# Performance work log

Measured on AMD Instinct MI355X. Metric: run time of the kernel, lower is better.

Reference implementation:

```python
import jax, jax.numpy as jnp
import numpy as np

N_NODES = 100000
N_EDGES = 3200000
IN_DIM = 128
HIDDEN = 64
N_GRAPHS = 512


def setup_inputs() -> dict:
    key = jax.random.key(0)
    k1, k2, k3, k4, k5, k6, k7, k8 = jax.random.split(key, 8)
    x = jax.random.normal(k1, (N_NODES, IN_DIM), dtype=jnp.float32)
    edge_index = jax.random.randint(k2, (2, N_EDGES), 0, N_NODES, dtype=jnp.int64)
    batch = jnp.sort(jax.random.randint(k3, (N_NODES,), 0, N_GRAPHS, dtype=jnp.int64))
    # Glorot-style init for GCNConv weights, zero bias (PyG default)
    s1 = 1.0 / np.sqrt(IN_DIM)
    s2 = 1.0 / np.sqrt(HIDDEN)
    W1 = jax.random.uniform(k4, (IN_DIM, HIDDEN), jnp.float32, -s1, s1)
    b1 = jnp.zeros((HIDDEN,), jnp.float32)
    W2 = jax.random.uniform(k5, (HIDDEN, HIDDEN), jnp.float32, -s2, s2)
    b2 = jnp.zeros((HIDDEN,), jnp.float32)
    return {"x": x, "W1": W1, "b1": b1, "W2": W2, "b2": b2,
            "edge_index": edge_index, "batch": batch}


def _gcn_conv(x, src, dst, W, b, n_nodes):
    # PyG GCNConv: h = x W;  out_i = sum_j norm_ij * h_j + b
    # with self-loops added and norm = deg^{-1/2}[src] * deg^{-1/2}[dst]
    h = x @ W  # [N, out]
    deg = jax.ops.segment_sum(jnp.ones_like(dst, dtype=h.dtype), dst,
                              num_segments=n_nodes)  # in-degree incl. self-loops
    dis = jnp.where(deg > 0, jax.lax.rsqrt(jnp.maximum(deg, 1e-12)), 0.0)
    norm = dis[src] * dis[dst]                      # [E+N]
    msg = h[src] * norm[:, None]                    # gather + scale
    out = jax.ops.segment_sum(msg, dst, num_segments=n_nodes)  # scatter-add
    return out + b


def reference(x, W1, b1, W2, b2, edge_index, batch):
    n = x.shape[0]
    loops = jnp.arange(n, dtype=edge_index.dtype)
    src = jnp.concatenate([edge_index[0], loops])
    dst = jnp.concatenate([edge_index[1], loops])
    h = jax.nn.relu(_gcn_conv(x, src, dst, W1, b1, n))
    h = jax.nn.relu(_gcn_conv(h, src, dst, W2, b2, n))
    # global_mean_pool over batch ids
    sums = jax.ops.segment_sum(h, batch, num_segments=N_GRAPHS)
    cnts = jax.ops.segment_sum(jnp.ones((n,), h.dtype), batch,
                               num_segments=N_GRAPHS)
    return sums / jnp.maximum(cnts, 1.0)[:, None]
```

## Files before the change

### kernel.cpp

```cpp
#include <hip/hip_runtime.h>
#include <hip/hip_bf16.h>

#define N_NODES 100000
#define N_EDGES 3200000
#define IN_DIM 128
#define HIDDEN 64
#define N_GRAPHS 512

#define NB 196
#define NPB 512
#define P1B 512
#define SEGC 80
#define BCAP2 18432

typedef __hip_bfloat16 bf16;
__device__ __forceinline__ float b2f(bf16 v) { return __bfloat162float(v); }

__global__ __launch_bounds__(512) void bin_kernel(const int* __restrict__ src,
                                                  const int* __restrict__ dst,
                                                  int* __restrict__ gcnt,
                                                  int* __restrict__ btot,
                                                  unsigned* __restrict__ slab) {
    __shared__ int lcnt[NB];
    int t = threadIdx.x, blk = blockIdx.x;
    if (t < NB) lcnt[t] = 0;
    __syncthreads();
    const int EPB = (N_EDGES + P1B - 1) / P1B;
    long e0 = (long)blk * EPB;
    long e1 = e0 + EPB; if (e1 > N_EDGES) e1 = N_EDGES;
    unsigned* ms = slab + (size_t)blk * NB * SEGC;
    for (long e = e0 + t; e < e1; e += 512) {
        int d = dst[e];
        unsigned p = ((unsigned)src[e] << 9) | (unsigned)(d & (NPB - 1));
        int bb = d >> 9;
        int pos = atomicAdd(&lcnt[bb], 1);
        if (pos < SEGC) ms[bb * SEGC + pos] = p;
    }
    __syncthreads();
    if (t < NB) {
        int c = lcnt[t]; if (c > SEGC) c = SEGC;
        gcnt[blk * NB + t] = c;
        atomicAdd(&btot[t], c);
    }
}

__global__ __launch_bounds__(256) void bstart_kernel(const int* __restrict__ btot,
                                                     int* __restrict__ bstart) {
    __shared__ int s[NB];
    int t = threadIdx.x;
    if (t < NB) s[t] = btot[t];
    __syncthreads();
    for (int off = 1; off < NB; off <<= 1) {
        int u = (t < NB && t >= off) ? s[t - off] : 0;
        __syncthreads();
        if (t < NB) s[t] += u;
        __syncthreads();
    }
    if (t < NB) bstart[t + 1] = s[t];
    if (t == 0) bstart[0] = 0;
}

__global__ __launch_bounds__(1024) void csr_sort_kernel(
        const unsigned* __restrict__ slab, const int* __restrict__ gcnt,
        const int* __restrict__ bstart, int2* __restrict__ be,
        float* __restrict__ dis, int* __restrict__ csr) {
    __shared__ int cnt[NPB], sc[NPB], lb[NPB], cur[NPB];
    __shared__ int stmp[P1B];
    __shared__ int segoff[P1B + 1];
    __shared__ unsigned ebuf[BCAP2];
    int b = blockIdx.x, t = threadIdx.x;
    if (t < P1B) stmp[t] = gcnt[t * NB + b];
    __syncthreads();
    for (int off = 1; off < P1B; off <<= 1) {
        int u = 0;
        if (t < P1B && t >= off) u = stmp[t - off];
        __syncthreads();
        if (t < P1B) stmp[t] += u;
        __syncthreads();
    }
    if (t < P1B) segoff[t + 1] = stmp[t];
    if (t == 0) segoff[0] = 0;
    __syncthreads();
    int ec = segoff[P1B];
    if (ec > BCAP2) ec = BCAP2;
    int w = t >> 6, lane = t & 63;
    for (int s = w; s < P1B; s += 16) {
        int o = segoff[s];
        int c = segoff[s + 1] - o;
        const unsigned* sp = slab + ((size_t)s * NB + b) * SEGC;
        for (int i = lane; i < c; i += 64)
            if (o + i < BCAP2) ebuf[o + i] = sp[i];
    }
    if (t < NPB) cnt[t] = 0;
    __syncthreads();
    for (int i = t; i < ec; i += 1024)
        atomicAdd(&cnt[(int)(ebuf[i] & (NPB - 1))], 1);
    __syncthreads();
    int v = (t < NPB) ? cnt[t] : 0;
    if (t < NPB) sc[t] = v;
    __syncthreads();
    for (int off = 1; off < NPB; off <<= 1) {
        int u = (t < NPB && t >= off) ? sc[t - off] : 0;
        __syncthreads();
        if (t < NPB) sc[t] += u;
        __syncthreads();
    }
    if (t < NPB) { lb[t] = sc[t] - v; cur[t] = 0; }
    __syncthreads();
    int gb0 = bstart[b];
    for (int i = t; i < ec; i += 1024) {
        unsigned p = ebuf[i];
        int dl = (int)(p & (NPB - 1));
        int k = atomicAdd(&cur[dl], 1);
        csr[gb0 + lb[dl] + k] = (int)(p >> 9);
    }
    int n0 = b * NPB;
    int nn = N_NODES - n0; if (nn > NPB) nn = NPB;
    if (t < nn) {
        int n = n0 + t;
        int bg = gb0 + lb[t];
        be[n] = make_int2(bg, bg + cnt[t]);
        dis[n] = rsqrtf((float)(cnt[t] + 1));
    }
}

template <int K>
__global__ __launch_bounds__(256) void gemm_kernel(
        const float* __restrict__ in, const float* __restrict__ W,
        const float* __restrict__ dis, bf16* __restrict__ hd) {
    int tid = threadIdx.x;
    int lane = tid & 63;
    float Wr[K];
    #pragma unroll
    for (int k = 0; k < K; ++k) Wr[k] = W[k * HIDDEN + lane];
    int w = __builtin_amdgcn_readfirstlane(tid >> 6);
    int wave = blockIdx.x * 4 + w;
    int nw = gridDim.x * 4;
    for (int n0 = wave * 4; n0 < N_NODES; n0 += nw * 4) {
        const float* xr = in + (size_t)n0 * K;
        float a0 = 0.f, a1 = 0.f, a2 = 0.f, a3 = 0.f;
        #pragma unroll
        for (int k = 0; k < K; ++k) {
            float wv = Wr[k];
            a0 = fmaf(xr[k],         wv, a0);
            a1 = fmaf(xr[K + k],     wv, a1);
            a2 = fmaf(xr[2 * K + k], wv, a2);
            a3 = fmaf(xr[3 * K + k], wv, a3);
        }
        bf16* o = hd + (size_t)n0 * HIDDEN + lane;
        o[0]          = __float2bfloat16(a0 * dis[n0]);
        o[HIDDEN]     = __float2bfloat16(a1 * dis[n0 + 1]);
        o[2 * HIDDEN] = __float2bfloat16(a2 * dis[n0 + 2]);
        o[3 * HIDDEN] = __float2bfloat16(a3 * dis[n0 + 3]);
    }
}

template <int POOL>
__global__ __launch_bounds__(256) void pull_kernel(
        const bf16* __restrict__ hd, const float* __restrict__ dis,
        const int2* __restrict__ be, const int* __restrict__ csr,
        const float* __restrict__ bias,
        float* __restrict__ act,
        const int* __restrict__ batch, float* __restrict__ pool,
        float* __restrict__ cnt) {
    int w = threadIdx.x >> 6, lane = threadIdx.x & 63;
    int wid = blockIdx.x * 4 + w;
    int nwaves = gridDim.x * 4;
    int per = (N_NODES + nwaves - 1) / nwaves;
    int n0 = wid * per;
    int n1 = n0 + per; if (n1 > N_NODES) n1 = N_NODES;
    for (int node = n0; node < n1; ++node) {
        int2 r = be[node];
        int beg = r.x, end = r.y;
        float a0 = 0.f, a1 = 0.f, a2 = 0.f, a3 = 0.f;
        for (int j = beg; j < end; j += 64) {
            int rem = end - j;
            int m = rem < 64 ? rem : 64;
            int idx = (lane < m) ? __builtin_nontemporal_load(&csr[j + lane]) : 0;
            int t = 0;
            for (; t + 8 <= m; t += 8) {
                int s0 = __shfl(idx, t);
                int s1 = __shfl(idx, t + 1);
                int s2 = __shfl(idx, t + 2);
                int s3 = __shfl(idx, t + 3);
                int s4 = __shfl(idx, t + 4);
                int s5 = __shfl(idx, t + 5);
                int s6 = __shfl(idx, t + 6);
                int s7 = __shfl(idx, t + 7);
                float v0 = b2f(hd[(size_t)s0 * HIDDEN + lane]);
                float v1 = b2f(hd[(size_t)s1 * HIDDEN + lane]);
                float v2 = b2f(hd[(size_t)s2 * HIDDEN + lane]);
                float v3 = b2f(hd[(size_t)s3 * HIDDEN + lane]);
                float v4 = b2f(hd[(size_t)s4 * HIDDEN + lane]);
                float v5 = b2f(hd[(size_t)s5 * HIDDEN + lane]);
                float v6 = b2f(hd[(size_t)s6 * HIDDEN + lane]);
                float v7 = b2f(hd[(size_t)s7 * HIDDEN + lane]);
                a0 += v0 + v4;
                a1 += v1 + v5;
                a2 += v2 + v6;
                a3 += v3 + v7;
            }
            for (; t < m; ++t) {
                int s = __shfl(idx, t);
                a0 += b2f(hd[(size_t)s * HIDDEN + lane]);
            }
        }
        float acc = (a0 + a1) + (a2 + a3);
        float self = b2f(hd[(size_t)node * HIDDEN + lane]);
        float row = dis[node] * (acc + self) + bias[lane];
        float v = row > 0.f ? row : 0.f;
        if (POOL == 0) {
            act[(size_t)node * HIDDEN + lane] = v;
        } else {
            int g = batch[node];
            atomicAdd(&pool[g * HIDDEN + lane], v);
            if (lane == 0) atomicAdd(&cnt[g], 1.0f);
        }
    }
}

__global__ void final_kernel(const float* __restrict__ pool,
                             const float* __restrict__ cnt,
                             float* __restrict__ out) {
    int i = blockIdx.x * blockDim.x + threadIdx.x;
    if (i < N_GRAPHS * HIDDEN) {
        float c = cnt[i >> 6];
        c = c > 1.0f ? c : 1.0f;
        out[i] = pool[i] / c;
    }
}

extern "C" void kernel_launch(void* const* d_in, const int* in_sizes, int n_in,
                              void* d_out, int out_size, void* d_ws, size_t ws_size,
                              hipStream_t stream) {
    const float* x  = (const float*)d_in[0];
    const float* W1 = (const float*)d_in[1];
    const float* b1 = (const float*)d_in[2];
    const float* W2 = (const float*)d_in[3];
    const float* b2 = (const float*)d_in[4];
    const int* edge_index = (const int*)d_in[5];
    const int* batch      = (const int*)d_in[6];
    float* out = (float*)d_out;
    (void)in_sizes; (void)n_in; (void)out_size; (void)ws_size;

    char* ws = (char*)d_ws;
    int*      gcnt   = (int*)     (ws + 0);
    int*      btot   = (int*)     (ws + 401408);
    int*      bstart = (int*)     (ws + 402432);
    float*    pool   = (float*)   (ws + 403456);
    float*    cnt    = (float*)   (ws + 534528);
    int2*     be     = (int2*)    (ws + 536576);
    float*    dis    = (float*)   (ws + 1336576);
    unsigned* slab   = (unsigned*)(ws + 1736704);
    float*    act    = (float*)   (ws + 1736704);
    int*      csr    = (int*)     (ws + 33849344);
    bf16*     hd     = (bf16*)    (ws + 46649344);

    const int* srcv = edge_index;
    const int* dstv = edge_index + N_EDGES;

    hipMemsetAsync(ws, 0, 536576, stream);

    bin_kernel<<<P1B, 512, 0, stream>>>(srcv, dstv, gcnt, btot, slab);
    bstart_kernel<<<1, 256, 0, stream>>>(btot, bstart);
    csr_sort_kernel<<<NB, 1024, 0, stream>>>(slab, gcnt, bstart, be, dis, csr);

    gemm_kernel<IN_DIM><<<1024, 256, 0, stream>>>(x, W1, dis, hd);
    pull_kernel<0><<<2048, 256, 0, stream>>>(hd, dis, be, csr, b1,
                                             act, nullptr, nullptr, nullptr);

    gemm_kernel<HIDDEN><<<1024, 256, 0, stream>>>(act, W2, dis, hd);
    pull_kernel<1><<<2048, 256, 0, stream>>>(hd, dis, be, csr, b2,
                                             nullptr, batch, pool, cnt);

    final_kernel<<<(N_GRAPHS * HIDDEN + 255) / 256, 256, 0, stream>>>(pool, cnt, out);
}
```

Measured before the change: 460.6 us.

## Fuse second-layer weight matmul into first GCN aggregation kernel

The first aggregation kernel now applies ReLU and then multiplies each node's row by W2, held in shared memory, using cross-lane readlane broadcasts. It writes the deg-scaled bf16 features for layer two directly. This eliminates the fp32 activation buffer write/read and the separate second GEMM launch. In exchange it adds per-node dot-product work and LDS usage to a gather-bound kernel, which may reduce occupancy.

Measured after the change: 486.7 us. 1.06x slower.

```diff
diff --git a/kernel.cpp b/kernel.cpp
--- a/kernel.cpp
+++ b/kernel.cpp
@@ -15,6 +15,9 @@
 
 typedef __hip_bfloat16 bf16;
 __device__ __forceinline__ float b2f(bf16 v) { return __bfloat162float(v); }
+__device__ __forceinline__ float rlane(float v, int k) {
+    return __int_as_float(__builtin_amdgcn_readlane(__float_as_int(v), k));
+}
 
 __global__ __launch_bounds__(512) void bin_kernel(const int* __restrict__ src,
                                                   const int* __restrict__ dst,
@@ -155,15 +158,17 @@
     }
 }
 
-template <int POOL>
-__global__ __launch_bounds__(256) void pull_kernel(
+__global__ __launch_bounds__(256) void pull_fused_kernel(
         const bf16* __restrict__ hd, const float* __restrict__ dis,
         const int2* __restrict__ be, const int* __restrict__ csr,
-        const float* __restrict__ bias,
-        float* __restrict__ act,
-        const int* __restrict__ batch, float* __restrict__ pool,
-        float* __restrict__ cnt) {
-    int w = threadIdx.x >> 6, lane = threadIdx.x & 63;
+        const float* __restrict__ bias, const float* __restrict__ W2,
+        bf16* __restrict__ hd2) {
+    __shared__ float W2s[HIDDEN * HIDDEN];
+    int t = threadIdx.x;
+    for (int i = t; i < HIDDEN * HIDDEN; i += 256) W2s[i] = W2[i];
+    __syncthreads();
+    int w = t >> 6, lane = t & 63;
+    float bl = bias[lane];
     int wid = blockIdx.x * 4 + w;
     int nwaves = gridDim.x * 4;
     int per = (N_NODES + nwaves - 1) / nwaves;
@@ -177,16 +182,16 @@
             int rem = end - j;
             int m = rem < 64 ? rem : 64;
             int idx = (lane < m) ? __builtin_nontemporal_load(&csr[j + lane]) : 0;
-            int t = 0;
-            for (; t + 8 <= m; t += 8) {
-                int s0 = __shfl(idx, t);
-                int s1 = __shfl(idx, t + 1);
-                int s2 = __shfl(idx, t + 2);
-                int s3 = __shfl(idx, t + 3);
-                int s4 = __shfl(idx, t + 4);
-                int s5 = __shfl(idx, t + 5);
-                int s6 = __shfl(idx, t + 6);
-                int s7 = __shfl(idx, t + 7);
+            int t8 = 0;
+            for (; t8 + 8 <= m; t8 += 8) {
+                int s0 = __shfl(idx, t8);
+                int s1 = __shfl(idx, t8 + 1);
+                int s2 = __shfl(idx, t8 + 2);
+                int s3 = __shfl(idx, t8 + 3);
+                int s4 = __shfl(idx, t8 + 4);
+                int s5 = __shfl(idx, t8 + 5);
+                int s6 = __shfl(idx, t8 + 6);
+                int s7 = __shfl(idx, t8 + 7);
                 float v0 = b2f(hd[(size_t)s0 * HIDDEN + lane]);
                 float v1 = b2f(hd[(size_t)s1 * HIDDEN + lane]);
                 float v2 = b2f(hd[(size_t)s2 * HIDDEN + lane]);
@@ -200,22 +205,80 @@
                 a2 += v2 + v6;
                 a3 += v3 + v7;
             }
-            for (; t < m; ++t) {
-                int s = __shfl(idx, t);
+            for (; t8 < m; ++t8) {
+                int s = __shfl(idx, t8);
+                a0 += b2f(hd[(size_t)s * HIDDEN + lane]);
+            }
+        }
+        float acc = (a0 + a1) + (a2 + a3);
+        float dn = dis[node];
+        float self = b2f(hd[(size_t)node * HIDDEN + lane]);
+        float row = dn * (acc + self) + bl;
+        float v = row > 0.f ? row : 0.f;
+        float g2 = 0.f;
+        #pragma unroll
+        for (int k = 0; k < HIDDEN; ++k)
+            g2 = fmaf(rlane(v, k), W2s[k * HIDDEN + lane], g2);
+        hd2[(size_t)node * HIDDEN + lane] = __float2bfloat16(g2 * dn);
+    }
+}
+
+__global__ __launch_bounds__(256) void pull_pool_kernel(
+        const bf16* __restrict__ hd, const float* __restrict__ dis,
+        const int2* __restrict__ be, const int* __restrict__ csr,
+        const float* __restrict__ bias,
+        const int* __restrict__ batch, float* __restrict__ pool,
+        float* __restrict__ cnt) {
+    int w = threadIdx.x >> 6, lane = threadIdx.x & 63;
+    float bl = bias[lane];
+    int wid = blockIdx.x * 4 + w;
+    int nwaves = gridDim.x * 4;
+    int per = (N_NODES + nwaves - 1) / nwaves;
+    int n0 = wid * per;
+    int n1 = n0 + per; if (n1 > N_NODES) n1 = N_NODES;
+    for (int node = n0; node < n1; ++node) {
+        int2 r = be[node];
+        int beg = r.x, end = r.y;
+        float a0 = 0.f, a1 = 0.f, a2 = 0.f, a3 = 0.f;
+        for (int j = beg; j < end; j += 64) {
+            int rem = end - j;
+            int m = rem < 64 ? rem : 64;
+            int idx = (lane < m) ? __builtin_nontemporal_load(&csr[j + lane]) : 0;
+            int t8 = 0;
+            for (; t8 + 8 <= m; t8 += 8) {
+                int s0 = __shfl(idx, t8);
+                int s1 = __shfl(idx, t8 + 1);
+                int s2 = __shfl(idx, t8 + 2);
+                int s3 = __shfl(idx, t8 + 3);
+                int s4 = __shfl(idx, t8 + 4);
+                int s5 = __shfl(idx, t8 + 5);
+                int s6 = __shfl(idx, t8 + 6);
+                int s7 = __shfl(idx, t8 + 7);
+                float v0 = b2f(hd[(size_t)s0 * HIDDEN + lane]);
+                float v1 = b2f(hd[(size_t)s1 * HIDDEN + lane]);
+                float v2 = b2f(hd[(size_t)s2 * HIDDEN + lane]);
+                float v3 = b2f(hd[(size_t)s3 * HIDDEN + lane]);
+                float v4 = b2f(hd[(size_t)s4 * HIDDEN + lane]);
+                float v5 = b2f(hd[(size_t)s5 * HIDDEN + lane]);
+                float v6 = b2f(hd[(size_t)s6 * HIDDEN + lane]);
+                float v7 = b2f(hd[(size_t)s7 * HIDDEN + lane]);
+                a0 += v0 + v4;
+                a1 += v1 + v5;
+                a2 += v2 + v6;
+                a3 += v3 + v7;
+            }
+            for (; t8 < m; ++t8) {
+                int s = __shfl(idx, t8);
                 a0 += b2f(hd[(size_t)s * HIDDEN + lane]);
             }
         }
         float acc = (a0 + a1) + (a2 + a3);
         float self = b2f(hd[(size_t)node * HIDDEN + lane]);
-        float row = dis[node] * (acc + self) + bias[lane];
+        float row = dis[node] * (acc + self) + bl;
         float v = row > 0.f ? row : 0.f;
-        if (POOL == 0) {
-            act[(size_t)node * HIDDEN + lane] = v;
-        } else {
-            int g = batch[node];
-            atomicAdd(&pool[g * HIDDEN + lane], v);
-            if (lane == 0) atomicAdd(&cnt[g], 1.0f);
-        }
+        int g = batch[node];
+        atomicAdd(&pool[g * HIDDEN + lane], v);
+        if (lane == 0) atomicAdd(&cnt[g], 1.0f);
     }
 }
 
@@ -252,9 +315,9 @@
     int2*     be     = (int2*)    (ws + 536576);
     float*    dis    = (float*)   (ws + 1336576);
     unsigned* slab   = (unsigned*)(ws + 1736704);
-    float*    act    = (float*)   (ws + 1736704);
+    bf16*     hd1    = (bf16*)    (ws + 1736704);
     int*      csr    = (int*)     (ws + 33849344);
-    bf16*     hd     = (bf16*)    (ws + 46649344);
+    bf16*     hd2    = (bf16*)    (ws + 46649344);
 
     const int* srcv = edge_index;
     const int* dstv = edge_index + N_EDGES;
@@ -265,13 +328,10 @@
     bstart_kernel<<<1, 256, 0, stream>>>(btot, bstart);
     csr_sort_kernel<<<NB, 1024, 0, stream>>>(slab, gcnt, bstart, be, dis, csr);
 
-    gemm_kernel<IN_DIM><<<1024, 256, 0, stream>>>(x, W1, dis, hd);
-    pull_kernel<0><<<2048, 256, 0, stream>>>(hd, dis, be, csr, b1,
-                                             act, nullptr, nullptr, nullptr);
-
-    gemm_kernel<HIDDEN><<<1024, 256, 0, stream>>>(act, W2, dis, hd);
-    pull_kernel<1><<<2048, 256, 0, stream>>>(hd, dis, be, csr, b2,
-                                             nullptr, batch, pool, cnt);
+    gemm_kernel<IN_DIM><<<1024, 256, 0, stream>>>(x, W1, dis, hd1);
+    pull_fused_kernel<<<2048, 256, 0, stream>>>(hd1, dis, be, csr, b1, W2, hd2);
+    pull_pool_kernel<<<2048, 256, 0, stream>>>(hd2, dis, be, csr, b2,
+                                               batch, pool, cnt);
 
     final_kernel<<<(N_GRAPHS * HIDDEN + 255) / 256, 256, 0, stream>>>(pool, cnt, out);
 }
```

## Split pull-kernel feature columns into two halves, each wave-half gathering alternate edges

Applied to the files above, without the earlier changes.

The pull aggregation now covers the 64 feature columns in two passes of 32. In each pass, the two 32-lane halves of a wave gather different neighbor edges at once and combine their sums with a cross-half shuffle. Each gather instruction therefore fetches two 64-byte bf16 row segments instead of one 128-byte row, which shrinks each pass's working set of hd and may improve L2 cache hit rates. In exchange, every node's CSR indices and row metadata are read twice, the instruction count roughly doubles, and each load moves less contiguous data.

After: 567.5 us. +23.2%, slower.

```diff
diff --git a/kernel.cpp b/kernel.cpp
--- a/kernel.cpp
+++ b/kernel.cpp
@@ -164,57 +164,75 @@
         const int* __restrict__ batch, float* __restrict__ pool,
         float* __restrict__ cnt) {
     int w = threadIdx.x >> 6, lane = threadIdx.x & 63;
+    int slot = lane >> 5;
+    int sub  = lane & 31;
     int wid = blockIdx.x * 4 + w;
     int nwaves = gridDim.x * 4;
     int per = (N_NODES + nwaves - 1) / nwaves;
     int n0 = wid * per;
     int n1 = n0 + per; if (n1 > N_NODES) n1 = N_NODES;
-    for (int node = n0; node < n1; ++node) {
-        int2 r = be[node];
-        int beg = r.x, end = r.y;
-        float a0 = 0.f, a1 = 0.f, a2 = 0.f, a3 = 0.f;
-        for (int j = beg; j < end; j += 64) {
-            int rem = end - j;
-            int m = rem < 64 ? rem : 64;
-            int idx = (lane < m) ? __builtin_nontemporal_load(&csr[j + lane]) : 0;
-            int t = 0;
-            for (; t + 8 <= m; t += 8) {
-                int s0 = __shfl(idx, t);
-                int s1 = __shfl(idx, t + 1);
-                int s2 = __shfl(idx, t + 2);
-                int s3 = __shfl(idx, t + 3);
-                int s4 = __shfl(idx, t + 4);
-                int s5 = __shfl(idx, t + 5);
-                int s6 = __shfl(idx, t + 6);
-                int s7 = __shfl(idx, t + 7);
-                float v0 = b2f(hd[(size_t)s0 * HIDDEN + lane]);
-                float v1 = b2f(hd[(size_t)s1 * HIDDEN + lane]);
-                float v2 = b2f(hd[(size_t)s2 * HIDDEN + lane]);
-                float v3 = b2f(hd[(size_t)s3 * HIDDEN + lane]);
-                float v4 = b2f(hd[(size_t)s4 * HIDDEN + lane]);
-                float v5 = b2f(hd[(size_t)s5 * HIDDEN + lane]);
-                float v6 = b2f(hd[(size_t)s6 * HIDDEN + lane]);
-                float v7 = b2f(hd[(size_t)s7 * HIDDEN + lane]);
-                a0 += v0 + v4;
-                a1 += v1 + v5;
-                a2 += v2 + v6;
-                a3 += v3 + v7;
+    for (int half = 0; half < 2; ++half) {
+        int fb = half * 32;
+        for (int node = n0; node < n1; ++node) {
+            int2 r = be[node];
+            int beg = r.x, end = r.y;
+            float a0 = 0.f, a1 = 0.f, a2 = 0.f, a3 = 0.f;
+            for (int j = beg; j < end; j += 64) {
+                int rem = end - j;
+                int m = rem < 64 ? rem : 64;
+                int idx = (lane < m) ? __builtin_nontemporal_load(&csr[j + lane]) : 0;
+                int t = 0;
+                for (; t + 16 <= m; t += 16) {
+                    int s0 = __shfl(idx, t + slot);
+                    int s1 = __shfl(idx, t + 2 + slot);
+                    int s2 = __shfl(idx, t + 4 + slot);
+                    int s3 = __shfl(idx, t + 6 + slot);
+                    int s4 = __shfl(idx, t + 8 + slot);
+                    int s5 = __shfl(idx, t + 10 + slot);
+                    int s6 = __shfl(idx, t + 12 + slot);
+                    int s7 = __shfl(idx, t + 14 + slot);
+                    float v0 = b2f(hd[(size_t)s0 * HIDDEN + fb + sub]);
+                    float v1 = b2f(hd[(size_t)s1 * HIDDEN + fb + sub]);
+                    float v2 = b2f(hd[(size_t)s2 * HIDDEN + fb + sub]);
+                    float v3 = b2f(hd[(size_t)s3 * HIDDEN + fb + sub]);
+                    float v4 = b2f(hd[(size_t)s4 * HIDDEN + fb + sub]);
+                    float v5 = b2f(hd[(size_t)s5 * HIDDEN + fb + sub]);
+                    float v6 = b2f(hd[(size_t)s6 * HIDDEN + fb + sub]);
+                    float v7 = b2f(hd[(size_t)s7 * HIDDEN + fb + sub]);
+                    a0 += v0 + v4;
+                    a1 += v1 + v5;
+                    a2 += v2 + v6;
+                    a3 += v3 + v7;
+                }
+                if (t < m) {
+                    #pragma unroll
+                    for (int u = 0; u < 8; ++u) {
+                        int eb = t + 2 * u;
+                        if (eb < m) {
+                            int e = eb + slot;
+                            int ee = e < 64 ? e : 63;
+                            int s = __shfl(idx, ee);
+                            float vv = b2f(hd[(size_t)s * HIDDEN + fb + sub]);
+                            if (e < m) a0 += vv;
+                        }
+                    }
+                }
             }
-            for (; t < m; ++t) {
-                int s = __shfl(idx, t);
-                a0 += b2f(hd[(size_t)s * HIDDEN + lane]);
+            float acc = (a0 + a1) + (a2 + a3);
+            acc += __shfl_xor(acc, 32);
+            float self = b2f(hd[(size_t)node * HIDDEN + fb + sub]);
+            float row = dis[node] * (acc + self) + bias[fb + sub];
+            float v = row > 0.f ? row : 0.f;
+            if (POOL == 0) {
+                if (slot == 0)
+                    act[(size_t)node * HIDDEN + fb + sub] = v;
+            } else {
+                if (slot == 0) {
+                    int g = batch[node];
+                    atomicAdd(&pool[g * HIDDEN + fb + sub], v);
+                    if (lane == 0 && half == 0) atomicAdd(&cnt[g], 1.0f);
+                }
             }
-        }
-        float acc = (a0 + a1) + (a2 + a3);
-        float self = b2f(hd[(size_t)node * HIDDEN + lane]);
-        float row = dis[node] * (acc + self) + bias[lane];
-        float v = row > 0.f ? row : 0.f;
-        if (POOL == 0) {
-            act[(size_t)node * HIDDEN + lane] = v;
-        } else {
-            int g = batch[node];
-            atomicAdd(&pool[g * HIDDEN + lane], v);
-            if (lane == 0) atomicAdd(&cnt[g], 1.0f);
         }
     }
 }
```
